# Kernel tuning notes

Hardware: AMD Instinct MI355X
Metric: run time of the kernel (lower is better)

The kernel has to match this reference:

```python
import jax, jax.numpy as jnp
import numpy as np

NZ, N_GEN = 128, 10
H1, H2, IMG = 512, 1024, 784
BATCH = 4096


def setup_inputs() -> dict:
    key = jax.random.key(0)
    ks = jax.random.split(key, 5)
    z = jax.random.normal(ks[0], (BATCH, NZ), dtype=jnp.float32)
    g_idx = jax.random.randint(ks[1], (BATCH,), 0, N_GEN)
    # stacked per-generator MLP weights (fan-in scaled init)
    W1 = jax.random.normal(ks[2], (N_GEN, NZ, H1), dtype=jnp.float32) / np.sqrt(NZ)
    b1 = jnp.zeros((N_GEN, H1), dtype=jnp.float32)
    W2 = jax.random.normal(ks[3], (N_GEN, H1, H2), dtype=jnp.float32) / np.sqrt(H1)
    b2 = jnp.zeros((N_GEN, H2), dtype=jnp.float32)
    W3 = jax.random.normal(ks[4], (N_GEN, H2, IMG), dtype=jnp.float32) / np.sqrt(H2)
    b3 = jnp.zeros((N_GEN, IMG), dtype=jnp.float32)
    return {"z": z, "g_idx": g_idx, "W1": W1, "b1": b1, "W2": W2, "b2": b2, "W3": W3, "b3": b3}


def reference(z, g_idx, W1, b1, W2, b2, W3, b3):
    # Run ALL n_gen sub-generators for every sample (as the torch module does),
    # then gather the chosen branch per sample.
    h = jax.nn.relu(jnp.einsum('bz,gzh->bgh', z, W1) + b1)          # [B, G, H1]
    h = jax.nn.relu(jnp.einsum('bgh,ghk->bgk', h, W2) + b2)         # [B, G, H2]
    images = jnp.tanh(jnp.einsum('bgk,gki->bgi', h, W3) + b3)       # [B, G, IMG]
    # images[arange(B), g_idx]
    out = jnp.take_along_axis(images, g_idx[:, None, None], axis=1)[:, 0]  # [B, IMG]
    return out
```

## Files before the change

### kernel.cpp

```cpp
#include <hip/hip_runtime.h>
#include <math.h>

#define NZ    128
#define H1    512
#define H2    1024
#define IMG   784
#define IMGP  896
#define BATCH 4096
#define NGEN  10
#define MPAD  128

typedef _Float16 f16;
typedef __attribute__((ext_vector_type(8))) _Float16 half8;
typedef __attribute__((ext_vector_type(4))) float floatx4;

#define TB1 ((NZ / 64) * (H1 / 64) * NGEN)
#define TB2 ((H1 / 64) * (H2 / 64) * NGEN)
#define TB3 ((H2 / 64) * (IMGP / 64) * NGEN)

#define NWG1 (8 * 4 * NGEN)
#define NWG2 (8 * 8 * NGEN)
#define NWG3 (8 * 7 * NGEN)

__device__ __forceinline__ void cp16(void* l, const void* g) {
    __builtin_amdgcn_global_load_lds((const __attribute__((address_space(1))) void*)g,
                                     (__attribute__((address_space(3))) void*)l, 16, 0, 0);
}

template<int K, int N, int NPAD>
__device__ void t_tile256(int idx, const float* __restrict__ W,
                          f16* __restrict__ Wt, f16 (*L)[72]) {
    constexpr int KT = K / 64, NTt = NPAD / 64;
    const int g  = idx / (KT * NTt);
    const int r2 = idx % (KT * NTt);
    const int k0 = (r2 % KT) * 64;
    const int n0 = (r2 / KT) * 64;
    const int t = threadIdx.x;
    {
        const int kk0 = t >> 4, nq = (t & 15) * 4;
        #pragma unroll
        for (int it = 0; it < 4; ++it) {
            const int kk = kk0 + it * 16;
            float4 v = make_float4(0.f, 0.f, 0.f, 0.f);
            if (n0 + nq < N)
                v = *(const float4*)(W + ((size_t)g * K + (k0 + kk)) * N + n0 + nq);
            L[nq + 0][kk] = (f16)v.x;
            L[nq + 1][kk] = (f16)v.y;
            L[nq + 2][kk] = (f16)v.z;
            L[nq + 3][kk] = (f16)v.w;
        }
    }
    __syncthreads();
    {
        const int nn0 = t >> 3, kq = (t & 7) * 8;
        #pragma unroll
        for (int it = 0; it < 2; ++it) {
            const int nn = nn0 + it * 32;
            *(half8*)(Wt + ((size_t)g * NPAD + (n0 + nn)) * K + k0 + kq) =
                *(const half8*)&L[nn][kq];
        }
    }
}

template<int K, int N, int NPAD>
__device__ void t_tile512(int idx, const float* __restrict__ W,
                          f16* __restrict__ Wt, char* smraw) {
    f16 (*L)[72] = (f16(*)[72])smraw;
    constexpr int KT = K / 64, NTt = NPAD / 64;
    const int g  = idx / (KT * NTt);
    const int r2 = idx % (KT * NTt);
    const int k0 = (r2 % KT) * 64;
    const int n0 = (r2 / KT) * 64;
    const int t = threadIdx.x;
    {
        const int kk0 = t >> 4;
        const int nq  = (t & 15) * 4;
        #pragma unroll
        for (int it = 0; it < 2; ++it) {
            const int kk = kk0 + it * 32;
            float4 v = make_float4(0.f, 0.f, 0.f, 0.f);
            if (n0 + nq < N)
                v = *(const float4*)(W + ((size_t)g * K + (k0 + kk)) * N + n0 + nq);
            L[nq + 0][kk] = (f16)v.x;
            L[nq + 1][kk] = (f16)v.y;
            L[nq + 2][kk] = (f16)v.z;
            L[nq + 3][kk] = (f16)v.w;
        }
    }
    __syncthreads();
    {
        const int nn = t >> 3, kq = (t & 7) * 8;
        *(half8*)(Wt + ((size_t)g * NPAD + (n0 + nn)) * K + k0 + kq) =
            *(const half8*)&L[nn][kq];
    }
}

__global__ __launch_bounds__(256)
void prep1(const float* __restrict__ W1, f16* __restrict__ W1t,
           const int* __restrict__ g_idx, int* __restrict__ seg,
           int* __restrict__ perm) {
    __shared__ f16 L[64][72];
    __shared__ int lc[NGEN];
    __shared__ int lb[NGEN + 1];
    const int bid = blockIdx.x;
    if (bid == 0) {
        const int t = threadIdx.x;
        if (t < NGEN) lc[t] = 0;
        __syncthreads();
        int gv[BATCH / 256];
        #pragma unroll
        for (int i = 0; i < BATCH / 256; ++i) {
            gv[i] = g_idx[t + i * 256];
            atomicAdd(&lc[gv[i]], 1);
        }
        __syncthreads();
        if (t == 0) {
            int s = 0;
            for (int g = 0; g < NGEN; ++g) { lb[g] = s; s += lc[g]; }
            lb[NGEN] = s;
        }
        __syncthreads();
        if (t <= NGEN) seg[t] = lb[t];
        if (t < NGEN) lc[t] = lb[t];
        __syncthreads();
        #pragma unroll
        for (int i = 0; i < BATCH / 256; ++i) {
            int p = atomicAdd(&lc[gv[i]], 1);
            perm[p] = t + i * 256;
        }
        return;
    }
    t_tile256<NZ, H1, H1>(bid - 1, W1, W1t, L);
}

template<int K, int NOUT, int NPADB, int NM, int NN, int ACT, int SCATTER>
__device__ void gemm8(int Lw, const f16* __restrict__ Ap,
                      const f16* __restrict__ Wt, const float* __restrict__ bias,
                      f16* __restrict__ Ch, float* __restrict__ Cout,
                      const int* __restrict__ seg, const int* __restrict__ perm,
                      char* smraw) {
    constexpr int NT = K / 64;
    const int g   = Lw / (NM * NN);
    const int rem = Lw - g * (NM * NN);
    const int nt  = rem / NM;
    const int mt0 = rem - nt * NM;
    const int s0 = seg[g];
    const int ng = seg[g + 1] - s0;
    const int m0 = mt0 * 128;
    if (m0 >= ng) return;
    const int n0 = nt * 128;

    f16* As = (f16*)smraw;
    f16* Bs = (f16*)(smraw + 32768);
    const int tid = threadIdx.x, lane = tid & 63, w = tid >> 6;

    const f16* ga[2]; const f16* gb[2]; int lo[2];
    #pragma unroll
    for (int j = 0; j < 2; ++j) {
        const int r   = w * 16 + j * 8 + (lane >> 3);
        const int swz = ((lane & 7) ^ ((r >> 1) & 7)) * 8;
        ga[j] = Ap + (size_t)(s0 + m0 + r) * K + swz;
        gb[j] = Wt + ((size_t)g * NPADB + n0 + r) * K + swz;
        lo[j] = (w * 16 + j * 8) * 64;
    }

    const int wm = (w & 1) * 64, wn = (w >> 1) * 32;
    const int lm = lane & 15, lq = lane >> 4;

    const int c = n0 + wn + 2 * lm;
    const bool in0 = (!SCATTER) || (c < NOUT);
    const float* bg = bias + (size_t)g * NOUT;
    const float bv0 = in0 ? bg[c]     : 0.f;
    const float bv1 = in0 ? bg[c + 1] : 0.f;

    floatx4 acc[4][2] = {};

    auto stage = [&](int t, int b) {
        #pragma unroll
        for (int j = 0; j < 2; ++j) cp16(&As[b * 8192 + lo[j]], ga[j] + (size_t)t * 64);
        #pragma unroll
        for (int j = 0; j < 2; ++j) cp16(&Bs[b * 8192 + lo[j]], gb[j] + (size_t)t * 64);
    };
    stage(0, 0);
    __builtin_amdgcn_sched_barrier(0);
    stage(1, 1);

    for (int kc = 0; kc < NT; ++kc) {
        if (kc + 1 < NT) asm volatile("s_waitcnt vmcnt(4)" ::: "memory");
        else             asm volatile("s_waitcnt vmcnt(0)" ::: "memory");
        __builtin_amdgcn_sched_barrier(0);
        __builtin_amdgcn_s_barrier();
        __builtin_amdgcn_sched_barrier(0);

        const int cb = (kc & 1) * 8192;
        half8 a[2][4], b[2][2];
        #pragma unroll
        for (int ks = 0; ks < 2; ++ks) {
            #pragma unroll
            for (int mt = 0; mt < 4; ++mt) {
                const int r  = wm + mt * 16 + lm;
                const int pq = (ks * 4 + lq) ^ ((r >> 1) & 7);
                a[ks][mt] = *(const half8*)&As[cb + r * 64 + pq * 8];
            }
            #pragma unroll
            for (int nf = 0; nf < 2; ++nf) {
                const int r  = wn + 2 * lm + nf;
                const int pq = (ks * 4 + lq) ^ ((r >> 1) & 7);
                b[ks][nf] = *(const half8*)&Bs[cb + r * 64 + pq * 8];
            }
        }
        asm volatile("s_waitcnt lgkmcnt(0)" ::: "memory");
        __builtin_amdgcn_sched_barrier(0);
        if (kc + 2 < NT) {
            __builtin_amdgcn_s_barrier();
            __builtin_amdgcn_sched_barrier(0);
            stage(kc + 2, kc & 1);
        }
        #pragma unroll
        for (int ks = 0; ks < 2; ++ks)
            #pragma unroll
            for (int mt = 0; mt < 4; ++mt)
                #pragma unroll
                for (int nf = 0; nf < 2; ++nf)
                    acc[mt][nf] = __builtin_amdgcn_mfma_f32_16x16x32_f16(
                        a[ks][mt], b[ks][nf], acc[mt][nf], 0, 0, 0);
    }

    #pragma unroll
    for (int mt = 0; mt < 4; ++mt)
        #pragma unroll
        for (int rr = 0; rr < 4; ++rr) {
            const int gr = m0 + wm + mt * 16 + lq * 4 + rr;
            if (gr >= ng) continue;
            float x0 = acc[mt][0][rr] + bv0;
            float x1 = acc[mt][1][rr] + bv1;
            if (ACT == 0) {
                x0 = fmaxf(x0, 0.f); x1 = fmaxf(x1, 0.f);
            } else {
                const float e0 = __expf(2.f * x0);
                const float e1 = __expf(2.f * x1);
                x0 = 1.f - 2.f / (e0 + 1.f);
                x1 = 1.f - 2.f / (e1 + 1.f);
            }
            if (SCATTER) {
                if (in0) {
                    const size_t orow = (size_t)perm[s0 + gr];
                    *(float2*)&Cout[orow * NOUT + c] = make_float2(x0, x1);
                }
            } else {
                union { uint u; f16 h[2]; } o;
                o.h[0] = (f16)x0; o.h[1] = (f16)x1;
                *(uint*)&Ch[(size_t)(s0 + gr) * NOUT + c] = o.u;
            }
        }
}

__device__ void l1_item(int Lw, const float* __restrict__ Az,
                        const f16* __restrict__ Wt, const float* __restrict__ bias,
                        f16* __restrict__ Ch, const int* __restrict__ seg,
                        const int* __restrict__ perm, char* smraw) {
    constexpr int K = NZ, NOUT = H1, NPADB = H1, NM = 8, NN = 4;
    const int g   = Lw / (NM * NN);
    const int rem = Lw - g * (NM * NN);
    const int nt  = rem / NM;
    const int mt0 = rem - nt * NM;
    const int s0 = seg[g];
    const int ng = seg[g + 1] - s0;
    const int m0 = mt0 * 128;
    if (m0 >= ng) return;
    const int n0 = nt * 128;

    f16* As = (f16*)smraw;
    f16* Bs = (f16*)(smraw + 32768);
    const int tid = threadIdx.x, lane = tid & 63, w = tid >> 6;

    #pragma unroll
    for (int j = 0; j < 2; ++j) {
        const int r   = w * 16 + j * 8 + (lane >> 3);
        const int swz = ((lane & 7) ^ ((r >> 1) & 7)) * 8;
        const f16* gbj = Wt + ((size_t)g * NPADB + n0 + r) * K + swz;
        const int  loj = (w * 16 + j * 8) * 64;
        cp16(&Bs[loj],        gbj);
        cp16(&Bs[8192 + loj], gbj + 64);
    }
    const int arow = tid >> 3, aq = tid & 7;
    #pragma unroll
    for (int p = 0; p < 2; ++p) {
        const int r   = arow + p * 64;
        const int prw = perm[min(s0 + m0 + r, BATCH - 1)];
        #pragma unroll
        for (int t = 0; t < 2; ++t) {
            const float* src = Az + (size_t)prw * K + t * 64 + aq * 8;
            const float4 v0 = *(const float4*)src;
            const float4 v1 = *(const float4*)(src + 4);
            half8 h;
            h[0] = (f16)v0.x; h[1] = (f16)v0.y; h[2] = (f16)v0.z; h[3] = (f16)v0.w;
            h[4] = (f16)v1.x; h[5] = (f16)v1.y; h[6] = (f16)v1.z; h[7] = (f16)v1.w;
            const int pq = aq ^ ((r >> 1) & 7);
            *(half8*)&As[t * 8192 + r * 64 + pq * 8] = h;
        }
    }

    const int wm = (w & 1) * 64, wn = (w >> 1) * 32;
    const int lm = lane & 15, lq = lane >> 4;
    const int c = n0 + wn + 2 * lm;
    const float* bg = bias + (size_t)g * NOUT;
    const float bv0 = bg[c], bv1 = bg[c + 1];

    __syncthreads();

    floatx4 acc[4][2] = {};
    #pragma unroll
    for (int kc = 0; kc < 2; ++kc) {
        const int cb = kc * 8192;
        half8 a[2][4], b[2][2];
        #pragma unroll
        for (int ks = 0; ks < 2; ++ks) {
            #pragma unroll
            for (int mt = 0; mt < 4; ++mt) {
                const int r  = wm + mt * 16 + lm;
                const int pq = (ks * 4 + lq) ^ ((r >> 1) & 7);
                a[ks][mt] = *(const half8*)&As[cb + r * 64 + pq * 8];
            }
            #pragma unroll
            for (int nf = 0; nf < 2; ++nf) {
                const int r  = wn + 2 * lm + nf;
                const int pq = (ks * 4 + lq) ^ ((r >> 1) & 7);
                b[ks][nf] = *(const half8*)&Bs[cb + r * 64 + pq * 8];
            }
        }
        #pragma unroll
        for (int ks = 0; ks < 2; ++ks)
            #pragma unroll
            for (int mt = 0; mt < 4; ++mt)
                #pragma unroll
                for (int nf = 0; nf < 2; ++nf)
                    acc[mt][nf] = __builtin_amdgcn_mfma_f32_16x16x32_f16(
                        a[ks][mt], b[ks][nf], acc[mt][nf], 0, 0, 0);
    }

    #pragma unroll
    for (int mt = 0; mt < 4; ++mt)
        #pragma unroll
        for (int rr = 0; rr < 4; ++rr) {
            const int gr = m0 + wm + mt * 16 + lq * 4 + rr;
            if (gr >= ng) continue;
            const float x0 = fmaxf(acc[mt][0][rr] + bv0, 0.f);
            const float x1 = fmaxf(acc[mt][1][rr] + bv1, 0.f);
            union { uint u; f16 h[2]; } o;
            o.h[0] = (f16)x0; o.h[1] = (f16)x1;
            *(uint*)&Ch[(size_t)(s0 + gr) * NOUT + c] = o.u;
        }
}

__global__ __launch_bounds__(512)
void l1f(const float* __restrict__ z, const f16* __restrict__ W1t,
         const float* __restrict__ b1, f16* __restrict__ h1p,
         const float* __restrict__ W2, f16* __restrict__ W2t,
         const int* __restrict__ seg, const int* __restrict__ perm) {
    __shared__ __align__(16) char sm[65536];
    const int bid = blockIdx.x;
    if (bid < NWG1) {
        const int Lw = (bid & 7) * (NWG1 / 8) + (bid >> 3);
        l1_item(Lw, z, W1t, b1, h1p, seg, perm, sm);
    } else {
        t_tile512<H1, H2, H2>(bid - NWG1, W2, W2t, sm);
    }
}

__global__ __launch_bounds__(512)
void g2f(const f16* __restrict__ h1p, const f16* __restrict__ W2t,
         const float* __restrict__ b2, f16* __restrict__ h2p,
         const float* __restrict__ W3, f16* __restrict__ W3t,
         const int* __restrict__ seg, const int* __restrict__ perm) {
    __shared__ __align__(16) char sm[65536];
    const int bid = blockIdx.x;
    if (bid < NWG2) {
        const int Lw = (bid & 7) * (NWG2 / 8) + (bid >> 3);
        gemm8<H1, H2, H2, 8, 8, 0, 0>(Lw, h1p, W2t, b2, h2p, nullptr,
                                      seg, perm, sm);
    } else {
        t_tile512<H2, IMG, IMGP>(bid - NWG2, W3, W3t, sm);
    }
}

__global__ __launch_bounds__(512)
void g3k(const f16* __restrict__ h2p, const f16* __restrict__ W3t,
         const float* __restrict__ b3, float* __restrict__ out,
         const int* __restrict__ seg, const int* __restrict__ perm) {
    __shared__ __align__(16) char sm[65536];
    const int bid = blockIdx.x;
    const int Lw = (bid & 7) * (NWG3 / 8) + (bid >> 3);
    gemm8<H2, IMG, IMGP, 8, 7, 1, 1>(Lw, h2p, W3t, b3, nullptr, out,
                                     seg, perm, sm);
}

extern "C" void kernel_launch(void* const* d_in, const int* in_sizes, int n_in,
                              void* d_out, int out_size, void* d_ws, size_t ws_size,
                              hipStream_t stream) {
    const float* z    = (const float*)d_in[0];
    const int*   gidx = (const int*)  d_in[1];
    const float* W1   = (const float*)d_in[2];
    const float* b1   = (const float*)d_in[3];
    const float* W2   = (const float*)d_in[4];
    const float* b2   = (const float*)d_in[5];
    const float* W3   = (const float*)d_in[6];
    const float* b3   = (const float*)d_in[7];
    float* out = (float*)d_out;

    char* ws = (char*)d_ws;
    size_t off = 0;
    auto alloc = [&](size_t bytes) { size_t o = off; off = (off + bytes + 255) & ~255ULL; return o; };
    int* seg  = (int*)(ws + alloc((size_t)(NGEN + 1) * 4));
    int* perm = (int*)(ws + alloc((size_t)(BATCH + MPAD) * 4));
    f16* h1p = (f16*)(ws + alloc((size_t)(BATCH + MPAD) * H1 * 2));
    f16* h2p = (f16*)(ws + alloc((size_t)(BATCH + MPAD) * H2 * 2));
    f16* W1t = (f16*)(ws + alloc((size_t)NGEN * H1 * NZ * 2));
    f16* W2t = (f16*)(ws + alloc((size_t)NGEN * H2 * H1 * 2));
    f16* W3t = (f16*)(ws + alloc((size_t)NGEN * IMGP * H2 * 2));

    prep1<<<dim3(1 + TB1), dim3(256), 0, stream>>>(W1, W1t, gidx, seg, perm);
    l1f<<<dim3(NWG1 + TB2), dim3(512), 0, stream>>>(z, W1t, b1, h1p, W2, W2t,
                                                    seg, perm);
    g2f<<<dim3(NWG2 + TB3), dim3(512), 0, stream>>>(h1p, W2t, b2, h2p, W3, W3t,
                                                    seg, perm);
    g3k<<<dim3(NWG3), dim3(512), 0, stream>>>(h2p, W3t, b3, out, seg, perm);
}
```

Measured before the change: 148.8 us.

## Triple-buffer LDS and double-buffer register fragments in grouped GEMM mainloop

The GEMM mainloop moves from a 2-stage LDS double buffer to a 3-stage ring. LDS fragment loads for the next k-step are now issued before the MFMAs of the current step run, with ping-pong register sets. MFMA blocks are wrapped in s_setprio, and one barrier per iteration is removed. LDS use rises to 96KB per block and register pressure grows, which may cut occupancy; the g1 layer still uses its own path.

```diff
diff --git a/kernel.cpp b/kernel.cpp
--- a/kernel.cpp
+++ b/kernel.cpp
@@ -140,6 +140,7 @@
                       const int* __restrict__ seg, const int* __restrict__ perm,
                       char* smraw) {
     constexpr int NT = K / 64;
+    static_assert(NT >= 4 && (NT & 1) == 0, "pipeline assumes even NT >= 4");
     const int g   = Lw / (NM * NN);
     const int rem = Lw - g * (NM * NN);
     const int nt  = rem / NM;
@@ -151,7 +152,7 @@
     const int n0 = nt * 128;
 
     f16* As = (f16*)smraw;
-    f16* Bs = (f16*)(smraw + 32768);
+    f16* Bs = (f16*)(smraw + 49152);
     const int tid = threadIdx.x, lane = tid & 63, w = tid >> 6;
 
     const f16* ga[2]; const f16* gb[2]; int lo[2];
@@ -174,6 +175,7 @@
     const float bv1 = in0 ? bg[c + 1] : 0.f;
 
     floatx4 acc[4][2] = {};
+    half8 uA[2][4], uB[2][2], vA[2][4], vB[2][2];
 
     auto stage = [&](int t, int b) {
         #pragma unroll
@@ -181,41 +183,25 @@
         #pragma unroll
         for (int j = 0; j < 2; ++j) cp16(&Bs[b * 8192 + lo[j]], gb[j] + (size_t)t * 64);
     };
-    stage(0, 0);
-    __builtin_amdgcn_sched_barrier(0);
-    stage(1, 1);
-
-    for (int kc = 0; kc < NT; ++kc) {
-        if (kc + 1 < NT) asm volatile("s_waitcnt vmcnt(4)" ::: "memory");
-        else             asm volatile("s_waitcnt vmcnt(0)" ::: "memory");
-        __builtin_amdgcn_sched_barrier(0);
-        __builtin_amdgcn_s_barrier();
-        __builtin_amdgcn_sched_barrier(0);
-
-        const int cb = (kc & 1) * 8192;
-        half8 a[2][4], b[2][2];
+    auto ldf = [&](int b3, half8 (&fa)[2][4], half8 (&fb)[2][2]) {
         #pragma unroll
         for (int ks = 0; ks < 2; ++ks) {
             #pragma unroll
             for (int mt = 0; mt < 4; ++mt) {
                 const int r  = wm + mt * 16 + lm;
                 const int pq = (ks * 4 + lq) ^ ((r >> 1) & 7);
-                a[ks][mt] = *(const half8*)&As[cb + r * 64 + pq * 8];
+                fa[ks][mt] = *(const half8*)&As[b3 * 8192 + r * 64 + pq * 8];
             }
             #pragma unroll
             for (int nf = 0; nf < 2; ++nf) {
                 const int r  = wn + 2 * lm + nf;
                 const int pq = (ks * 4 + lq) ^ ((r >> 1) & 7);
-                b[ks][nf] = *(const half8*)&Bs[cb + r * 64 + pq * 8];
-            }
-        }
-        asm volatile("s_waitcnt lgkmcnt(0)" ::: "memory");
-        __builtin_amdgcn_sched_barrier(0);
-        if (kc + 2 < NT) {
-            __builtin_amdgcn_s_barrier();
-            __builtin_amdgcn_sched_barrier(0);
-            stage(kc + 2, kc & 1);
-        }
+                fb[ks][nf] = *(const half8*)&Bs[b3 * 8192 + r * 64 + pq * 8];
+            }
+        }
+    };
+    auto domf = [&](half8 (&fa)[2][4], half8 (&fb)[2][2]) {
+        __builtin_amdgcn_s_setprio(1);
         #pragma unroll
         for (int ks = 0; ks < 2; ++ks)
             #pragma unroll
@@ -223,7 +209,51 @@
                 #pragma unroll
                 for (int nf = 0; nf < 2; ++nf)
                     acc[mt][nf] = __builtin_amdgcn_mfma_f32_16x16x32_f16(
-                        a[ks][mt], b[ks][nf], acc[mt][nf], 0, 0, 0);
+                        fa[ks][mt], fb[ks][nf], acc[mt][nf], 0, 0, 0);
+        __builtin_amdgcn_s_setprio(0);
+    };
+    auto stepk = [&](int kc, int cur, int nxt,
+                     half8 (&ua)[2][4], half8 (&ub)[2][2],
+                     half8 (&la)[2][4], half8 (&lb)[2][2]) {
+        if (kc + 3 < NT) stage(kc + 3, cur);
+        if (kc + 1 < NT) ldf(nxt, la, lb);
+        __builtin_amdgcn_sched_barrier(0);
+        domf(ua, ub);
+        asm volatile("s_waitcnt lgkmcnt(0)" ::: "memory");
+        __builtin_amdgcn_sched_barrier(0);
+        if (kc + 2 < NT) {
+            if (kc + 3 < NT) asm volatile("s_waitcnt vmcnt(4)" ::: "memory");
+            else             asm volatile("s_waitcnt vmcnt(0)" ::: "memory");
+            __builtin_amdgcn_sched_barrier(0);
+        }
+        if (kc + 1 < NT) {
+            __builtin_amdgcn_s_barrier();
+            __builtin_amdgcn_sched_barrier(0);
+        }
+    };
+
+    stage(0, 0);
+    __builtin_amdgcn_sched_barrier(0);
+    stage(1, 1);
+    __builtin_amdgcn_sched_barrier(0);
+    stage(2, 2);
+    asm volatile("s_waitcnt vmcnt(4)" ::: "memory");
+    __builtin_amdgcn_sched_barrier(0);
+    __builtin_amdgcn_s_barrier();
+    __builtin_amdgcn_sched_barrier(0);
+    ldf(0, uA, uB);
+    asm volatile("s_waitcnt lgkmcnt(0)" ::: "memory");
+    __builtin_amdgcn_sched_barrier(0);
+    __builtin_amdgcn_s_barrier();
+    __builtin_amdgcn_sched_barrier(0);
+
+    int cur = 0;
+    for (int kc = 0; kc < NT; kc += 2) {
+        const int n1 = (cur >= 2) ? cur - 2 : cur + 1;
+        stepk(kc,     cur, n1, uA, uB, vA, vB);
+        const int n2 = (n1 >= 2) ? n1 - 2 : n1 + 1;
+        stepk(kc + 1, n1,  n2, vA, vB, uA, uB);
+        cur = n2;
     }
 
     #pragma unroll
@@ -373,7 +403,7 @@
          const float* __restrict__ b2, f16* __restrict__ h2p,
          const float* __restrict__ W3, f16* __restrict__ W3t,
          const int* __restrict__ seg, const int* __restrict__ perm) {
-    __shared__ __align__(16) char sm[65536];
+    __shared__ __align__(16) char sm[98304];
     const int bid = blockIdx.x;
     if (bid < NWG2) {
         const int Lw = (bid & 7) * (NWG2 / 8) + (bid >> 3);
@@ -388,7 +418,7 @@
 void g3k(const f16* __restrict__ h2p, const f16* __restrict__ W3t,
          const float* __restrict__ b3, float* __restrict__ out,
          const int* __restrict__ seg, const int* __restrict__ perm) {
-    __shared__ __align__(16) char sm[65536];
+    __shared__ __align__(16) char sm[98304];
     const int bid = blockIdx.x;
     const int Lw = (bid & 7) * (NWG3 / 8) + (bid >> 3);
     gemm8<H2, IMG, IMGP, 8, 7, 1, 1>(Lw, h2p, W3t, b3, nullptr, out,
```

Result: slower. 160.7 us (+8.0%).
